# Optimization experiments

Measured on AMD Instinct MI355X. Metric: run time of the kernel, lower is better.

Reference implementation:

```python
import jax, jax.numpy as jnp
import numpy as np

H = 256  # hidden_dim


def _mlp(x, w1, b1, w2, b2):
    # Linear -> ReLU -> (Dropout=identity in eval) -> Linear
    return jax.nn.relu(x @ w1 + b1) @ w2 + b2


def setup_inputs() -> dict:
    key = jax.random.key(0)
    ks = jax.random.split(key, 9)
    bsz, seq = 32, 4096
    s = 1.0 / np.sqrt(2 * H)
    inp = {
        "h": jax.random.normal(ks[0], (bsz, seq, H), dtype=jnp.float32),
        "mask": jnp.ones((bsz, seq), dtype=jnp.float32),
        "ew1": jax.random.uniform(ks[1], (2 * H, H), minval=-s, maxval=s),
        "eb1": jax.random.uniform(ks[2], (H,), minval=-s, maxval=s),
        "ew2": jax.random.uniform(ks[3], (H, H), minval=-s, maxval=s),
        "eb2": jax.random.uniform(ks[4], (H,), minval=-s, maxval=s),
        "nw1": jax.random.uniform(ks[5], (2 * H, H), minval=-s, maxval=s),
        "nb1": jax.random.uniform(ks[6], (H,), minval=-s, maxval=s),
        "nw2": jax.random.uniform(ks[7], (H, H), minval=-s, maxval=s),
        "nb2": jax.random.uniform(ks[8], (H,), minval=-s, maxval=s),
    }
    return inp


def reference(h, mask, ew1, eb1, ew2, eb2, nw1, nb1, nw2, nb2):
    left = h[:, :-1, :]   # [B, S-1, H]
    right = h[:, 1:, :]   # [B, S-1, H]
    m_lr = _mlp(jnp.concatenate([left, right], axis=-1), ew1, eb1, ew2, eb2)
    m_rl = _mlp(jnp.concatenate([right, left], axis=-1), ew1, eb1, ew2, eb2)
    # shifted scatter-add: agg[:,1:] += m_lr ; agg[:,:-1] += m_rl
    zcol = jnp.zeros_like(h[:, :1, :])
    agg = jnp.concatenate([zcol, m_lr], axis=1) + jnp.concatenate([m_rl, zcol], axis=1)
    updated = _mlp(jnp.concatenate([h, agg], axis=-1), nw1, nb1, nw2, nb2)
    updated = updated * mask[:, :, None]
    return h + updated
```

## Files before the change

### kernel.cpp

```cpp
#include <hip/hip_runtime.h>
#include <hip/hip_bf16.h>

typedef __bf16 bf16_t;
typedef bf16_t bf16x8 __attribute__((ext_vector_type(8)));
typedef bf16_t bf16x4 __attribute__((ext_vector_type(4)));
typedef float f32x4 __attribute__((ext_vector_type(4)));

#define SEQ 4096
#define BSZ 32
#define T_TOK 64
#define PROWS 66
#define LSTR 264

#define OFF_P0 0
#define OFF_P1 (PROWS * LSTR)
#define OFF_P2 (2 * PROWS * LSTR)
#define SMEM_ELEMS (3 * PROWS * LSTR)
#define SMEM_BYTES (SMEM_ELEMS * 2)

#define W1F 0
#define NAF 131072
#define WBF 196608
#define N2F 262144
#define B2N 327680

#define BAR() asm volatile("s_waitcnt lgkmcnt(0)\n\ts_barrier" ::: "memory")

__global__ void wprep(const float* __restrict__ ew1, const float* __restrict__ nw1,
                      const float* __restrict__ nw2, bf16_t* __restrict__ wsw) {
    int idx = blockIdx.x * 256 + threadIdx.x;
    int region, rel, outbase;
    if (idx < 131072)      { region = 0; rel = idx;          outbase = W1F; }
    else if (idx < 196608) { region = 1; rel = idx - 131072; outbase = NAF; }
    else                   { region = 2; rel = idx - 196608; outbase = N2F; }
    int f = rel >> 9, o = rel & 511;
    int l = o >> 3, e = o & 7;
    int r = l & 15, kg = l >> 4;
    int nt = f >> 3, ks = f & 7;
    int k = ks * 32 + kg * 8 + e;
    int n = nt * 16 + r;
    float v;
    if (region == 0)
        v = (nt < 16) ? ew1[k * 256 + n] : ew1[(256 + k) * 256 + (n - 256)];
    else if (region == 1)
        v = nw1[k * 256 + n];
    else
        v = nw2[k * 256 + n];
    wsw[outbase + rel] = (bf16_t)v;
}

__global__ void wprep2(const float* __restrict__ ew2, const float* __restrict__ eb2,
                       const float* __restrict__ nw1, bf16_t* __restrict__ wsw) {
    int k = blockIdx.x;
    int n = threadIdx.x;
    if (k < 256) {
        float acc = 0.f;
        for (int j = 0; j < 256; ++j)
            acc += ew2[k * 256 + j] * nw1[(256 + j) * 256 + n];
        int ks = k >> 5, kg = (k >> 3) & 3, e = k & 7;
        int nt = n >> 4, r = n & 15;
        wsw[WBF + ((nt * 8 + ks) << 9) + ((kg * 16 + r) << 3) + e] = (bf16_t)acc;
    } else {
        float acc = 0.f;
        for (int j = 0; j < 256; ++j)
            acc += eb2[j] * nw1[(256 + j) * 256 + n];
        ((float*)(wsw + B2N))[n] = acc;
    }
}

__launch_bounds__(512, 2)
__global__ void gnl_kernel(const float* __restrict__ h, const float* __restrict__ mask,
                           const float* __restrict__ eb1, const float* __restrict__ nb1,
                           const float* __restrict__ nb2,
                           const bf16_t* __restrict__ wsw, float* __restrict__ out) {
    extern __shared__ bf16_t sm[];

    const int tid   = threadIdx.x;
    const int lane  = tid & 63;
    const int w     = tid >> 6;
    const int batch = blockIdx.x >> 6;
    const int tile  = blockIdx.x & 63;
    const int t0    = tile * T_TOK;
    const long baseTok = (long)batch * SEQ;

    const int c   = lane & 15;
    const int kg  = lane >> 4;
    const int crb = kg << 2;
    const int n0a = w * 16;
    const int n0b = (w + 8) * 16;

    auto loadw = [&](bf16x8 (&f)[8], int base, int nt) {
#pragma unroll
        for (int ks = 0; ks < 8; ++ks)
            f[ks] = *(const bf16x8*)(wsw + base + ((nt * 8 + ks) << 9) + (lane << 3));
    };
    auto loada = [&](bf16x8 (&f)[8], int poff, int rbase) {
        const bf16_t* p = sm + poff + (rbase + c) * LSTR + (kg << 3);
#pragma unroll
        for (int ks = 0; ks < 8; ++ks) f[ks] = *(const bf16x8*)(p + (ks << 5));
    };
    auto mfma2 = [&](bf16x8 (&f)[8], bf16x8 (&wa)[8], bf16x8 (&wb)[8],
                     f32x4& a0, f32x4& a1) {
        __builtin_amdgcn_s_setprio(1);
#pragma unroll
        for (int ks = 0; ks < 8; ++ks) {
            a0 = __builtin_amdgcn_mfma_f32_16x16x32_bf16(wa[ks], f[ks], a0, 0, 0, 0);
            a1 = __builtin_amdgcn_mfma_f32_16x16x32_bf16(wb[ks], f[ks], a1, 0, 0, 0);
        }
        __builtin_amdgcn_s_setprio(0);
    };

    for (int cc = tid; cc < PROWS * 32; cc += 512) {
        int r = cc >> 5;
        int fc = (cc & 31) << 3;
        int t = t0 - 1 + r;
        bf16x8 vals;
        if (t >= 0 && t < SEQ) {
            const float* src = h + (((long)(baseTok + t)) << 8) + fc;
            float4 x0 = ((const float4*)src)[0];
            float4 x1 = ((const float4*)src)[1];
            vals[0] = (bf16_t)x0.x; vals[1] = (bf16_t)x0.y;
            vals[2] = (bf16_t)x0.z; vals[3] = (bf16_t)x0.w;
            vals[4] = (bf16_t)x1.x; vals[5] = (bf16_t)x1.y;
            vals[6] = (bf16_t)x1.z; vals[7] = (bf16_t)x1.w;
        } else {
#pragma unroll
            for (int j = 0; j < 8; ++j) vals[j] = (bf16_t)0.0f;
        }
        *(bf16x8*)(sm + OFF_P0 + r * LSTR + fc) = vals;
    }
    BAR();

#pragma unroll
    for (int p = 0; p < 2; ++p) {
        bf16x8 wa[8], wb[8];
        loadw(wa, W1F, w + p * 16);
        loadw(wb, W1F, w + p * 16 + 8);
        int poff = p ? OFF_P2 : OFF_P1;
        bf16x8 fA[8], fB[8];
        loada(fA, OFF_P0, 0);
#pragma unroll
        for (int mt = 0; mt < 5; ++mt) {
            bf16x8 (&cur)[8] = (mt & 1) ? fB : fA;
            bf16x8 (&nxt)[8] = (mt & 1) ? fA : fB;
            if (mt < 4) loada(nxt, OFF_P0, (mt + 1) * 16);
            f32x4 aA = {0.f, 0.f, 0.f, 0.f}, aB = {0.f, 0.f, 0.f, 0.f};
            mfma2(cur, wa, wb, aA, aB);
            int row = mt * 16 + c;
            if (row < PROWS) {
                bf16x4 pA, pB;
#pragma unroll
                for (int j = 0; j < 4; ++j) { pA[j] = (bf16_t)aA[j]; pB[j] = (bf16_t)aB[j]; }
                *(bf16x4*)(sm + poff + row * LSTR + n0a + crb) = pA;
                *(bf16x4*)(sm + poff + row * LSTR + n0b + crb) = pB;
            }
        }
    }

    f32x4 ha[4][2];
    {
        bf16x8 na[8], nb8[8];
        loadw(na, NAF, w);
        loadw(nb8, NAF, w + 8);
        bf16x8 fA[8], fB[8];
        loada(fA, OFF_P0, 1);
#pragma unroll
        for (int tm = 0; tm < 4; ++tm) {
            bf16x8 (&cur)[8] = (tm & 1) ? fB : fA;
            bf16x8 (&nxt)[8] = (tm & 1) ? fA : fB;
            if (tm < 3) loada(nxt, OFF_P0, tm * 16 + 17);
            f32x4 a0 = {0.f, 0.f, 0.f, 0.f}, a1 = {0.f, 0.f, 0.f, 0.f};
            mfma2(cur, na, nb8, a0, a1);
            ha[tm][0] = a0; ha[tm][1] = a1;
        }
    }

    bf16x8 wba[8], wbb[8];
    loadw(wba, WBF, w);
    loadw(wbb, WBF, w + 8);
    BAR();

#pragma unroll
    for (int it = 0; it < 4; ++it) {
        int cc = tid + it * 512;
        int i = cc >> 5;
        int fc = (cc & 31) << 3;
        float bl = (t0 + i >= 1) ? 1.f : 0.f;
        float br = (t0 + i <= SEQ - 2) ? 1.f : 0.f;
        bf16x8 aL = *(const bf16x8*)(sm + OFF_P1 + i * LSTR + fc);
        bf16x8 aR = *(const bf16x8*)(sm + OFF_P1 + (i + 2) * LSTR + fc);
        bf16x8 bC = *(const bf16x8*)(sm + OFF_P2 + (i + 1) * LSTR + fc);
        float4 b1a = *(const float4*)(eb1 + fc);
        float4 b1b = *(const float4*)(eb1 + fc + 4);
        bf16x8 sv;
#pragma unroll
        for (int j = 0; j < 8; ++j) {
            float b1f = (j < 4) ? ((const float*)&b1a)[j] : ((const float*)&b1b)[j - 4];
            float x = (float)bC[j] + b1f;
            float l = fmaxf((float)aL[j] + x, 0.f) * bl;
            float r = fmaxf((float)aR[j] + x, 0.f) * br;
            sv[j] = (bf16_t)(l + r);
        }
        *(bf16x8*)(sm + OFF_P0 + i * LSTR + fc) = sv;
    }
    BAR();

    {
        float4 n1a = *(const float4*)(nb1 + n0a + crb);
        float4 n1b = *(const float4*)(nb1 + n0b + crb);
        const float* b2n = (const float*)(wsw + B2N);
        float4 c2a = *(const float4*)(b2n + n0a + crb);
        float4 c2b = *(const float4*)(b2n + n0b + crb);
        bf16x8 fA[8], fB[8];
        loada(fA, OFF_P0, 0);
#pragma unroll
        for (int tm = 0; tm < 4; ++tm) {
            bf16x8 (&cur)[8] = (tm & 1) ? fB : fA;
            bf16x8 (&nxt)[8] = (tm & 1) ? fA : fB;
            if (tm < 3) loada(nxt, OFF_P0, (tm + 1) * 16);
            f32x4 a0 = ha[tm][0], a1 = ha[tm][1];
            mfma2(cur, wba, wbb, a0, a1);
            int row = tm * 16 + c;
            int t = t0 + row;
            float cnt = ((t >= 1) ? 1.f : 0.f) + ((t <= SEQ - 2) ? 1.f : 0.f);
            bf16x4 p0, p1;
#pragma unroll
            for (int j = 0; j < 4; ++j) {
                p0[j] = (bf16_t)fmaxf(a0[j] + ((const float*)&n1a)[j] + cnt * ((const float*)&c2a)[j], 0.f);
                p1[j] = (bf16_t)fmaxf(a1[j] + ((const float*)&n1b)[j] + cnt * ((const float*)&c2b)[j], 0.f);
            }
            *(bf16x4*)(sm + OFF_P1 + row * LSTR + n0a + crb) = p0;
            *(bf16x4*)(sm + OFF_P1 + row * LSTR + n0b + crb) = p1;
        }
    }
    bf16x8 n2a[8], n2b[8];
    loadw(n2a, N2F, w);
    loadw(n2b, N2F, w + 8);
    BAR();

    {
        float4 v2a = *(const float4*)(nb2 + n0a + crb);
        float4 v2b = *(const float4*)(nb2 + n0b + crb);
        bf16x8 fA[8], fB[8];
        loada(fA, OFF_P1, 0);
#pragma unroll
        for (int tm = 0; tm < 4; ++tm) {
            long t = baseTok + t0 + tm * 16 + c;
            float m = mask[t];
            long g0 = (t << 8) + n0a + crb;
            long g1 = (t << 8) + n0b + crb;
            float4 h0 = *(const float4*)(h + g0);
            float4 h1 = *(const float4*)(h + g1);
            bf16x8 (&cur)[8] = (tm & 1) ? fB : fA;
            bf16x8 (&nxt)[8] = (tm & 1) ? fA : fB;
            if (tm < 3) loada(nxt, OFF_P1, (tm + 1) * 16);
            f32x4 a0 = {0.f, 0.f, 0.f, 0.f}, a1 = {0.f, 0.f, 0.f, 0.f};
            mfma2(cur, n2a, n2b, a0, a1);
            float4 o0, o1;
            o0.x = h0.x + m * (a0[0] + v2a.x);
            o0.y = h0.y + m * (a0[1] + v2a.y);
            o0.z = h0.z + m * (a0[2] + v2a.z);
            o0.w = h0.w + m * (a0[3] + v2a.w);
            o1.x = h1.x + m * (a1[0] + v2b.x);
            o1.y = h1.y + m * (a1[1] + v2b.y);
            o1.z = h1.z + m * (a1[2] + v2b.z);
            o1.w = h1.w + m * (a1[3] + v2b.w);
            *(float4*)(out + g0) = o0;
            *(float4*)(out + g1) = o1;
        }
    }
}

extern "C" void kernel_launch(void* const* d_in, const int* in_sizes, int n_in,
                              void* d_out, int out_size, void* d_ws, size_t ws_size,
                              hipStream_t stream) {
    const float* h    = (const float*)d_in[0];
    const float* mask = (const float*)d_in[1];
    const float* ew1  = (const float*)d_in[2];
    const float* eb1  = (const float*)d_in[3];
    const float* ew2  = (const float*)d_in[4];
    const float* eb2  = (const float*)d_in[5];
    const float* nw1  = (const float*)d_in[6];
    const float* nb1  = (const float*)d_in[7];
    const float* nw2  = (const float*)d_in[8];
    const float* nb2  = (const float*)d_in[9];
    float* out   = (float*)d_out;
    bf16_t* wsw  = (bf16_t*)d_ws;

    wprep<<<1024, 256, 0, stream>>>(ew1, nw1, nw2, wsw);
    wprep2<<<257, 256, 0, stream>>>(ew2, eb2, nw1, wsw);

    hipFuncSetAttribute(reinterpret_cast<const void*>(gnl_kernel),
                        hipFuncAttributeMaxDynamicSharedMemorySize, SMEM_BYTES);

    gnl_kernel<<<BSZ * (SEQ / T_TOK), 512, SMEM_BYTES, stream>>>(
        h, mask, eb1, nb1, nb2, wsw, out);
}
```

Measured before the change: 169.5 us.

## Make blocks loop over eight tiles with a double-buffered, prefetched h panel

The grid shrinks from 2048 blocks to 256, and each block walks eight consecutive 64-token tiles of one sequence. Two shared-memory h panels alternate between tiles. The next tile's h rows are loaded into registers before the final GEMM and written to shared memory after it, so global load latency overlaps with compute. The residual add now reads h from the bf16 shared panel instead of re-reading fp32 h from global memory, which removes a second global read of h but lowers the residual's precision to bf16. Shared memory grows to four panels, and with only 256 blocks the kernel relies on one block per CU keeping the device busy.

Result: slower. 256.5 us (+51.3%).

```diff
diff --git a/kernel.cpp b/kernel.cpp
--- a/kernel.cpp
+++ b/kernel.cpp
@@ -11,11 +11,13 @@
 #define T_TOK 64
 #define PROWS 66
 #define LSTR 264
-
-#define OFF_P0 0
-#define OFF_P1 (PROWS * LSTR)
-#define OFF_P2 (2 * PROWS * LSTR)
-#define SMEM_ELEMS (3 * PROWS * LSTR)
+#define NPANEL (PROWS * LSTR)
+
+#define OFF_X0 0
+#define OFF_X1 NPANEL
+#define OFF_A  (2 * NPANEL)
+#define OFF_B  (3 * NPANEL)
+#define SMEM_ELEMS (4 * NPANEL)
 #define SMEM_BYTES (SMEM_ELEMS * 2)
 
 #define W1F 0
@@ -78,9 +80,8 @@
     const int tid   = threadIdx.x;
     const int lane  = tid & 63;
     const int w     = tid >> 6;
-    const int batch = blockIdx.x >> 6;
-    const int tile  = blockIdx.x & 63;
-    const int t0    = tile * T_TOK;
+    const int batch = blockIdx.x >> 3;
+    const int tcb   = (blockIdx.x & 7) * 8;
     const long baseTok = (long)batch * SEQ;
 
     const int c   = lane & 15;
@@ -89,10 +90,10 @@
     const int n0a = w * 16;
     const int n0b = (w + 8) * 16;
 
-    auto loadw = [&](bf16x8 (&f)[8], int base, int nt) {
+    auto loadw = [&](bf16x8 (&f)[8], const bf16_t* wp, int base, int nt) {
 #pragma unroll
         for (int ks = 0; ks < 8; ++ks)
-            f[ks] = *(const bf16x8*)(wsw + base + ((nt * 8 + ks) << 9) + (lane << 3));
+            f[ks] = *(const bf16x8*)(wp + base + ((nt * 8 + ks) << 9) + (lane << 3));
     };
     auto loada = [&](bf16x8 (&f)[8], int poff, int rbase) {
         const bf16_t* p = sm + poff + (rbase + c) * LSTR + (kg << 3);
@@ -110,164 +111,219 @@
         __builtin_amdgcn_s_setprio(0);
     };
 
-    for (int cc = tid; cc < PROWS * 32; cc += 512) {
-        int r = cc >> 5;
-        int fc = (cc & 31) << 3;
-        int t = t0 - 1 + r;
-        bf16x8 vals;
-        if (t >= 0 && t < SEQ) {
-            const float* src = h + (((long)(baseTok + t)) << 8) + fc;
-            float4 x0 = ((const float4*)src)[0];
-            float4 x1 = ((const float4*)src)[1];
-            vals[0] = (bf16_t)x0.x; vals[1] = (bf16_t)x0.y;
-            vals[2] = (bf16_t)x0.z; vals[3] = (bf16_t)x0.w;
-            vals[4] = (bf16_t)x1.x; vals[5] = (bf16_t)x1.y;
-            vals[6] = (bf16_t)x1.z; vals[7] = (bf16_t)x1.w;
-        } else {
-#pragma unroll
-            for (int j = 0; j < 8; ++j) vals[j] = (bf16_t)0.0f;
-        }
-        *(bf16x8*)(sm + OFF_P0 + r * LSTR + fc) = vals;
+    {
+        const int t00 = tcb * T_TOK;
+#pragma unroll
+        for (int k = 0; k < 5; ++k) {
+            int cc = tid + k * 512;
+            if (cc < PROWS * 32) {
+                int r = cc >> 5, fc = (cc & 31) << 3;
+                int t = t00 - 1 + r;
+                bf16x8 v;
+                if (t >= 0 && t < SEQ) {
+                    const float* src = h + (((long)(baseTok + t)) << 8) + fc;
+                    float4 x0 = ((const float4*)src)[0];
+                    float4 x1 = ((const float4*)src)[1];
+                    v[0] = (bf16_t)x0.x; v[1] = (bf16_t)x0.y;
+                    v[2] = (bf16_t)x0.z; v[3] = (bf16_t)x0.w;
+                    v[4] = (bf16_t)x1.x; v[5] = (bf16_t)x1.y;
+                    v[6] = (bf16_t)x1.z; v[7] = (bf16_t)x1.w;
+                } else {
+#pragma unroll
+                    for (int q = 0; q < 8; ++q) v[q] = (bf16_t)0.0f;
+                }
+                *(bf16x8*)(sm + OFF_X0 + r * LSTR + fc) = v;
+            }
+        }
     }
     BAR();
 
-#pragma unroll
-    for (int p = 0; p < 2; ++p) {
-        bf16x8 wa[8], wb[8];
-        loadw(wa, W1F, w + p * 16);
-        loadw(wb, W1F, w + p * 16 + 8);
-        int poff = p ? OFF_P2 : OFF_P1;
-        bf16x8 fA[8], fB[8];
-        loada(fA, OFF_P0, 0);
-#pragma unroll
-        for (int mt = 0; mt < 5; ++mt) {
-            bf16x8 (&cur)[8] = (mt & 1) ? fB : fA;
-            bf16x8 (&nxt)[8] = (mt & 1) ? fA : fB;
-            if (mt < 4) loada(nxt, OFF_P0, (mt + 1) * 16);
-            f32x4 aA = {0.f, 0.f, 0.f, 0.f}, aB = {0.f, 0.f, 0.f, 0.f};
-            mfma2(cur, wa, wb, aA, aB);
-            int row = mt * 16 + c;
-            if (row < PROWS) {
-                bf16x4 pA, pB;
-#pragma unroll
-                for (int j = 0; j < 4; ++j) { pA[j] = (bf16_t)aA[j]; pB[j] = (bf16_t)aB[j]; }
-                *(bf16x4*)(sm + poff + row * LSTR + n0a + crb) = pA;
-                *(bf16x4*)(sm + poff + row * LSTR + n0b + crb) = pB;
-            }
-        }
-    }
-
-    f32x4 ha[4][2];
-    {
-        bf16x8 na[8], nb8[8];
-        loadw(na, NAF, w);
-        loadw(nb8, NAF, w + 8);
-        bf16x8 fA[8], fB[8];
-        loada(fA, OFF_P0, 1);
-#pragma unroll
-        for (int tm = 0; tm < 4; ++tm) {
-            bf16x8 (&cur)[8] = (tm & 1) ? fB : fA;
-            bf16x8 (&nxt)[8] = (tm & 1) ? fA : fB;
-            if (tm < 3) loada(nxt, OFF_P0, tm * 16 + 17);
-            f32x4 a0 = {0.f, 0.f, 0.f, 0.f}, a1 = {0.f, 0.f, 0.f, 0.f};
-            mfma2(cur, na, nb8, a0, a1);
-            ha[tm][0] = a0; ha[tm][1] = a1;
-        }
-    }
-
-    bf16x8 wba[8], wbb[8];
-    loadw(wba, WBF, w);
-    loadw(wbb, WBF, w + 8);
-    BAR();
-
-#pragma unroll
-    for (int it = 0; it < 4; ++it) {
-        int cc = tid + it * 512;
-        int i = cc >> 5;
-        int fc = (cc & 31) << 3;
-        float bl = (t0 + i >= 1) ? 1.f : 0.f;
-        float br = (t0 + i <= SEQ - 2) ? 1.f : 0.f;
-        bf16x8 aL = *(const bf16x8*)(sm + OFF_P1 + i * LSTR + fc);
-        bf16x8 aR = *(const bf16x8*)(sm + OFF_P1 + (i + 2) * LSTR + fc);
-        bf16x8 bC = *(const bf16x8*)(sm + OFF_P2 + (i + 1) * LSTR + fc);
-        float4 b1a = *(const float4*)(eb1 + fc);
-        float4 b1b = *(const float4*)(eb1 + fc + 4);
-        bf16x8 sv;
-#pragma unroll
-        for (int j = 0; j < 8; ++j) {
-            float b1f = (j < 4) ? ((const float*)&b1a)[j] : ((const float*)&b1b)[j - 4];
-            float x = (float)bC[j] + b1f;
-            float l = fmaxf((float)aL[j] + x, 0.f) * bl;
-            float r = fmaxf((float)aR[j] + x, 0.f) * br;
-            sv[j] = (bf16_t)(l + r);
-        }
-        *(bf16x8*)(sm + OFF_P0 + i * LSTR + fc) = sv;
-    }
-    BAR();
-
-    {
-        float4 n1a = *(const float4*)(nb1 + n0a + crb);
-        float4 n1b = *(const float4*)(nb1 + n0b + crb);
-        const float* b2n = (const float*)(wsw + B2N);
-        float4 c2a = *(const float4*)(b2n + n0a + crb);
-        float4 c2b = *(const float4*)(b2n + n0b + crb);
-        bf16x8 fA[8], fB[8];
-        loada(fA, OFF_P0, 0);
-#pragma unroll
-        for (int tm = 0; tm < 4; ++tm) {
-            bf16x8 (&cur)[8] = (tm & 1) ? fB : fA;
-            bf16x8 (&nxt)[8] = (tm & 1) ? fA : fB;
-            if (tm < 3) loada(nxt, OFF_P0, (tm + 1) * 16);
-            f32x4 a0 = ha[tm][0], a1 = ha[tm][1];
-            mfma2(cur, wba, wbb, a0, a1);
-            int row = tm * 16 + c;
-            int t = t0 + row;
-            float cnt = ((t >= 1) ? 1.f : 0.f) + ((t <= SEQ - 2) ? 1.f : 0.f);
-            bf16x4 p0, p1;
-#pragma unroll
-            for (int j = 0; j < 4; ++j) {
-                p0[j] = (bf16_t)fmaxf(a0[j] + ((const float*)&n1a)[j] + cnt * ((const float*)&c2a)[j], 0.f);
-                p1[j] = (bf16_t)fmaxf(a1[j] + ((const float*)&n1b)[j] + cnt * ((const float*)&c2b)[j], 0.f);
-            }
-            *(bf16x4*)(sm + OFF_P1 + row * LSTR + n0a + crb) = p0;
-            *(bf16x4*)(sm + OFF_P1 + row * LSTR + n0b + crb) = p1;
-        }
-    }
-    bf16x8 n2a[8], n2b[8];
-    loadw(n2a, N2F, w);
-    loadw(n2b, N2F, w + 8);
-    BAR();
-
-    {
-        float4 v2a = *(const float4*)(nb2 + n0a + crb);
-        float4 v2b = *(const float4*)(nb2 + n0b + crb);
-        bf16x8 fA[8], fB[8];
-        loada(fA, OFF_P1, 0);
-#pragma unroll
-        for (int tm = 0; tm < 4; ++tm) {
-            long t = baseTok + t0 + tm * 16 + c;
-            float m = mask[t];
-            long g0 = (t << 8) + n0a + crb;
-            long g1 = (t << 8) + n0b + crb;
-            float4 h0 = *(const float4*)(h + g0);
-            float4 h1 = *(const float4*)(h + g1);
-            bf16x8 (&cur)[8] = (tm & 1) ? fB : fA;
-            bf16x8 (&nxt)[8] = (tm & 1) ? fA : fB;
-            if (tm < 3) loada(nxt, OFF_P1, (tm + 1) * 16);
-            f32x4 a0 = {0.f, 0.f, 0.f, 0.f}, a1 = {0.f, 0.f, 0.f, 0.f};
-            mfma2(cur, n2a, n2b, a0, a1);
-            float4 o0, o1;
-            o0.x = h0.x + m * (a0[0] + v2a.x);
-            o0.y = h0.y + m * (a0[1] + v2a.y);
-            o0.z = h0.z + m * (a0[2] + v2a.z);
-            o0.w = h0.w + m * (a0[3] + v2a.w);
-            o1.x = h1.x + m * (a1[0] + v2b.x);
-            o1.y = h1.y + m * (a1[1] + v2b.y);
-            o1.z = h1.z + m * (a1[2] + v2b.z);
-            o1.w = h1.w + m * (a1[3] + v2b.w);
-            *(float4*)(out + g0) = o0;
-            *(float4*)(out + g1) = o1;
-        }
+    for (int j = 0; j < 8; ++j) {
+        const bf16_t* wsw_ = wsw;
+        asm volatile("" : "+s"(wsw_));
+        const int t0 = (tcb + j) * T_TOK;
+        const int hb = (j & 1) ? OFF_X1 : OFF_X0;
+        const int sp = (j & 1) ? OFF_X0 : OFF_X1;
+
+#pragma unroll
+        for (int p = 0; p < 2; ++p) {
+            bf16x8 wa[8], wb[8];
+            loadw(wa, wsw_, W1F, w + p * 16);
+            loadw(wb, wsw_, W1F, w + p * 16 + 8);
+            int poff = p ? OFF_B : OFF_A;
+            bf16x8 fA[8], fB[8];
+            loada(fA, hb, 0);
+#pragma unroll
+            for (int mt = 0; mt < 5; ++mt) {
+                bf16x8 (&cur)[8] = (mt & 1) ? fB : fA;
+                bf16x8 (&nxt)[8] = (mt & 1) ? fA : fB;
+                if (mt < 4) loada(nxt, hb, (mt + 1) * 16);
+                f32x4 aA = {0.f, 0.f, 0.f, 0.f}, aB = {0.f, 0.f, 0.f, 0.f};
+                mfma2(cur, wa, wb, aA, aB);
+                int row = mt * 16 + c;
+                if (row < PROWS) {
+                    bf16x4 pA, pB;
+#pragma unroll
+                    for (int q = 0; q < 4; ++q) { pA[q] = (bf16_t)aA[q]; pB[q] = (bf16_t)aB[q]; }
+                    *(bf16x4*)(sm + poff + row * LSTR + n0a + crb) = pA;
+                    *(bf16x4*)(sm + poff + row * LSTR + n0b + crb) = pB;
+                }
+            }
+        }
+
+        f32x4 ha[4][2];
+        {
+            bf16x8 na[8], nb8[8];
+            loadw(na, wsw_, NAF, w);
+            loadw(nb8, wsw_, NAF, w + 8);
+            bf16x8 fA[8], fB[8];
+            loada(fA, hb, 1);
+#pragma unroll
+            for (int tm = 0; tm < 4; ++tm) {
+                bf16x8 (&cur)[8] = (tm & 1) ? fB : fA;
+                bf16x8 (&nxt)[8] = (tm & 1) ? fA : fB;
+                if (tm < 3) loada(nxt, hb, tm * 16 + 17);
+                f32x4 a0 = {0.f, 0.f, 0.f, 0.f}, a1 = {0.f, 0.f, 0.f, 0.f};
+                mfma2(cur, na, nb8, a0, a1);
+                ha[tm][0] = a0; ha[tm][1] = a1;
+            }
+        }
+
+        bf16x8 wba[8], wbb[8];
+        loadw(wba, wsw_, WBF, w);
+        loadw(wbb, wsw_, WBF, w + 8);
+        BAR();
+
+#pragma unroll
+        for (int it = 0; it < 4; ++it) {
+            int cc = tid + it * 512;
+            int i = cc >> 5;
+            int fc = (cc & 31) << 3;
+            float bl = (t0 + i >= 1) ? 1.f : 0.f;
+            float br = (t0 + i <= SEQ - 2) ? 1.f : 0.f;
+            bf16x8 aL = *(const bf16x8*)(sm + OFF_A + i * LSTR + fc);
+            bf16x8 aR = *(const bf16x8*)(sm + OFF_A + (i + 2) * LSTR + fc);
+            bf16x8 bC = *(const bf16x8*)(sm + OFF_B + (i + 1) * LSTR + fc);
+            float4 b1a = *(const float4*)(eb1 + fc);
+            float4 b1b = *(const float4*)(eb1 + fc + 4);
+            bf16x8 sv;
+#pragma unroll
+            for (int q = 0; q < 8; ++q) {
+                float b1f = (q < 4) ? ((const float*)&b1a)[q] : ((const float*)&b1b)[q - 4];
+                float x = (float)bC[q] + b1f;
+                float l = fmaxf((float)aL[q] + x, 0.f) * bl;
+                float r = fmaxf((float)aR[q] + x, 0.f) * br;
+                sv[q] = (bf16_t)(l + r);
+            }
+            *(bf16x8*)(sm + sp + i * LSTR + fc) = sv;
+        }
+        BAR();
+
+        {
+            float4 n1a = *(const float4*)(nb1 + n0a + crb);
+            float4 n1b = *(const float4*)(nb1 + n0b + crb);
+            const float* b2n = (const float*)(wsw_ + B2N);
+            float4 c2a = *(const float4*)(b2n + n0a + crb);
+            float4 c2b = *(const float4*)(b2n + n0b + crb);
+            bf16x8 fA[8], fB[8];
+            loada(fA, sp, 0);
+#pragma unroll
+            for (int tm = 0; tm < 4; ++tm) {
+                bf16x8 (&cur)[8] = (tm & 1) ? fB : fA;
+                bf16x8 (&nxt)[8] = (tm & 1) ? fA : fB;
+                if (tm < 3) loada(nxt, sp, (tm + 1) * 16);
+                f32x4 a0 = ha[tm][0], a1 = ha[tm][1];
+                mfma2(cur, wba, wbb, a0, a1);
+                int row = tm * 16 + c;
+                int t = t0 + row;
+                float cnt = ((t >= 1) ? 1.f : 0.f) + ((t <= SEQ - 2) ? 1.f : 0.f);
+                bf16x4 p0, p1;
+#pragma unroll
+                for (int q = 0; q < 4; ++q) {
+                    p0[q] = (bf16_t)fmaxf(a0[q] + ((const float*)&n1a)[q] + cnt * ((const float*)&c2a)[q], 0.f);
+                    p1[q] = (bf16_t)fmaxf(a1[q] + ((const float*)&n1b)[q] + cnt * ((const float*)&c2b)[q], 0.f);
+                }
+                *(bf16x4*)(sm + OFF_A + row * LSTR + n0a + crb) = p0;
+                *(bf16x4*)(sm + OFF_A + row * LSTR + n0b + crb) = p1;
+            }
+        }
+        bf16x8 n2a[8], n2b[8];
+        loadw(n2a, wsw_, N2F, w);
+        loadw(n2b, wsw_, N2F, w + 8);
+        BAR();
+
+        const int nt0 = (tcb + j + 1) * T_TOK;
+        float4 s0[5], s1[5];
+        if (j < 7) {
+#pragma unroll
+            for (int k = 0; k < 5; ++k) {
+                int cc = tid + k * 512;
+                if (cc < PROWS * 32) {
+                    int r = cc >> 5, fc = (cc & 31) << 3;
+                    int t = nt0 - 1 + r;
+                    int tc = (t < 0) ? 0 : ((t > SEQ - 1) ? SEQ - 1 : t);
+                    const float* src = h + (((long)(baseTok + tc)) << 8) + fc;
+                    s0[k] = ((const float4*)src)[0];
+                    s1[k] = ((const float4*)src)[1];
+                }
+            }
+        }
+
+        {
+            float4 v2a = *(const float4*)(nb2 + n0a + crb);
+            float4 v2b = *(const float4*)(nb2 + n0b + crb);
+            bf16x8 fA[8], fB[8];
+            loada(fA, OFF_A, 0);
+#pragma unroll
+            for (int tm = 0; tm < 4; ++tm) {
+                long t = baseTok + t0 + tm * 16 + c;
+                float m = mask[t];
+                bf16x8 (&cur)[8] = (tm & 1) ? fB : fA;
+                bf16x8 (&nxt)[8] = (tm & 1) ? fA : fB;
+                if (tm < 3) loada(nxt, OFF_A, (tm + 1) * 16);
+                f32x4 a0 = {0.f, 0.f, 0.f, 0.f}, a1 = {0.f, 0.f, 0.f, 0.f};
+                mfma2(cur, n2a, n2b, a0, a1);
+                int rrow = tm * 16 + c + 1;
+                bf16x4 r0 = *(const bf16x4*)(sm + hb + rrow * LSTR + n0a + crb);
+                bf16x4 r1 = *(const bf16x4*)(sm + hb + rrow * LSTR + n0b + crb);
+                long g0 = (t << 8) + n0a + crb;
+                long g1 = (t << 8) + n0b + crb;
+                float4 o0, o1;
+                o0.x = (float)r0[0] + m * (a0[0] + v2a.x);
+                o0.y = (float)r0[1] + m * (a0[1] + v2a.y);
+                o0.z = (float)r0[2] + m * (a0[2] + v2a.z);
+                o0.w = (float)r0[3] + m * (a0[3] + v2a.w);
+                o1.x = (float)r1[0] + m * (a1[0] + v2b.x);
+                o1.y = (float)r1[1] + m * (a1[1] + v2b.y);
+                o1.z = (float)r1[2] + m * (a1[2] + v2b.z);
+                o1.w = (float)r1[3] + m * (a1[3] + v2b.w);
+                *(float4*)(out + g0) = o0;
+                *(float4*)(out + g1) = o1;
+            }
+        }
+
+        if (j < 7) {
+#pragma unroll
+            for (int k = 0; k < 5; ++k) {
+                int cc = tid + k * 512;
+                if (cc < PROWS * 32) {
+                    int r = cc >> 5, fc = (cc & 31) << 3;
+                    int t = nt0 - 1 + r;
+                    bf16x8 v;
+                    if (t >= 0 && t < SEQ) {
+                        v[0] = (bf16_t)s0[k].x; v[1] = (bf16_t)s0[k].y;
+                        v[2] = (bf16_t)s0[k].z; v[3] = (bf16_t)s0[k].w;
+                        v[4] = (bf16_t)s1[k].x; v[5] = (bf16_t)s1[k].y;
+                        v[6] = (bf16_t)s1[k].z; v[7] = (bf16_t)s1[k].w;
+                    } else {
+#pragma unroll
+                        for (int q = 0; q < 8; ++q) v[q] = (bf16_t)0.0f;
+                    }
+                    *(bf16x8*)(sm + sp + r * LSTR + fc) = v;
+                }
+            }
+        }
+        BAR();
     }
 }
 
@@ -293,6 +349,6 @@
     hipFuncSetAttribute(reinterpret_cast<const void*>(gnl_kernel),
                         hipFuncAttributeMaxDynamicSharedMemorySize, SMEM_BYTES);
 
-    gnl_kernel<<<BSZ * (SEQ / T_TOK), 512, SMEM_BYTES, stream>>>(
+    gnl_kernel<<<256, 512, SMEM_BYTES, stream>>>(
         h, mask, eb1, nb1, nb2, wsw, out);
 }
```
